# Optimization experiments

Hardware: AMD Instinct MI355X
Metric: run time of the kernel (lower is better)

## Reference

```python
import jax, jax.numpy as jnp
import numpy as np

N = 20000
E = 320000
LN_EPS = 1e-5
NEG_SLOPE = 0.2


def setup_inputs() -> dict:
    key = jax.random.key(0)
    ks = jax.random.split(key, 12)
    d = {}
    d['x'] = jax.random.normal(ks[0], (N, 512), dtype=jnp.float32)
    d['edge_index'] = jax.random.randint(ks[1], (2, E), 0, N, dtype=jnp.int64)
    s = 1.0 / np.sqrt(512.0)
    d['W1'] = jax.random.normal(ks[2], (512, 512), dtype=jnp.float32) * s
    d['a_src1'] = jax.random.normal(ks[3], (8, 64), dtype=jnp.float32) * s
    d['a_dst1'] = jax.random.normal(ks[4], (8, 64), dtype=jnp.float32) * s
    d['b1'] = jnp.zeros((512,), jnp.float32)
    d['g1'] = jnp.ones((512,), jnp.float32)
    d['beta1'] = jnp.zeros((512,), jnp.float32)
    d['W2'] = jax.random.normal(ks[5], (512, 512), dtype=jnp.float32) * s
    d['a_src2'] = jax.random.normal(ks[6], (1, 512), dtype=jnp.float32) * s
    d['a_dst2'] = jax.random.normal(ks[7], (1, 512), dtype=jnp.float32) * s
    d['b2'] = jnp.zeros((512,), jnp.float32)
    d['g2'] = jnp.ones((512,), jnp.float32)
    d['beta2'] = jnp.zeros((512,), jnp.float32)
    return d


def _segment_softmax(logits, seg, num_segments):
    # logits: [E, H]; softmax over edges sharing the same destination node
    m = jax.ops.segment_max(logits, seg, num_segments=num_segments)  # [N, H]
    e = jnp.exp(logits - m[seg])
    s = jax.ops.segment_sum(e, seg, num_segments=num_segments)  # [N, H]
    return e / s[seg]


def _gat_conv(x, src, dst, W, a_s, a_d, b, concat):
    # PyG GATConv (eval mode, self-loops already appended to src/dst)
    H, C = a_s.shape
    n = x.shape[0]
    h = (x @ W).reshape(n, H, C)                      # [N, H, C]
    alpha_s = jnp.einsum('nhc,hc->nh', h, a_s)        # [N, H]
    alpha_d = jnp.einsum('nhc,hc->nh', h, a_d)
    logits = jax.nn.leaky_relu(alpha_s[src] + alpha_d[dst], NEG_SLOPE)  # [E, H]
    alpha = _segment_softmax(logits, dst, n)          # [E, H]
    msg = h[src] * alpha[:, :, None]                  # [E, H, C]
    out = jax.ops.segment_sum(msg, dst, num_segments=n)  # [N, H, C]
    out = out.reshape(n, H * C) if concat else out.mean(axis=1)
    return out + b


def _layer_norm(x, g, beta):
    mu = jnp.mean(x, axis=-1, keepdims=True)
    var = jnp.var(x, axis=-1, keepdims=True)
    return (x - mu) * jax.lax.rsqrt(var + LN_EPS) * g + beta


def _forward(x, edge_index, W1, a_src1, a_dst1, b1, g1, beta1,
             W2, a_src2, a_dst2, b2, g2, beta2):
    n = x.shape[0]
    loops = jnp.arange(n, dtype=edge_index.dtype)
    src = jnp.concatenate([edge_index[0], loops])
    dst = jnp.concatenate([edge_index[1], loops])
    # layer 1: heads=8, concat
    x_new = _gat_conv(x, src, dst, W1, a_src1, a_dst1, b1, concat=True)
    x_new = jax.nn.elu(_layer_norm(x_new, g1, beta1))
    x = x + x_new  # 512 == 512 residual
    # layer 2: heads=1, mean (concat=False)
    x_new = _gat_conv(x, src, dst, W2, a_src2, a_dst2, b2, concat=False)
    x_new = jax.nn.elu(_layer_norm(x_new, g2, beta2))
    return x + x_new


def reference(x, edge_index, W1, a_src1, a_dst1, b1, g1, beta1,
              W2, a_src2, a_dst2, b2, g2, beta2):
    return _forward(x, edge_index, W1, a_src1, a_dst1, b1, g1, beta1,
                    W2, a_src2, a_dst2, b2, g2, beta2)
```

## Files before the change

kernel.cpp:

```cpp
#include <hip/hip_runtime.h>
#include <hip/hip_bf16.h>
#include <math.h>

#define NN 20000
#define NE 320000
#define DIM 512
#define LN_EPS 1e-5f
#define NEG_SLOPE 0.2f

typedef __attribute__((ext_vector_type(8))) short bf16x8;
typedef __attribute__((ext_vector_type(4))) float f32x4;
typedef __attribute__((ext_vector_type(4))) unsigned int u32x4;

__device__ inline void gload_lds16(const void* g, void* l) {
    __builtin_amdgcn_global_load_lds(
        (const __attribute__((address_space(1))) void*)g,
        (__attribute__((address_space(3))) void*)l, 16, 0, 0);
}

__device__ inline short f2bf(float f) {
    __hip_bfloat16 b = __float2bfloat16(f);
    return *reinterpret_cast<short*>(&b);
}


__global__ void count_k(const int* __restrict__ dst, int* __restrict__ cnt) {
    int e = blockIdx.x * blockDim.x + threadIdx.x;
    if (e < NE) {
        int d = dst[e];
        d = (d < 0) ? 0 : (d >= NN ? NN - 1 : d);
        atomicAdd(&cnt[d], 1);
    }
}

__global__ __launch_bounds__(1024) void scan_k(const int* __restrict__ cnt,
                                               int* __restrict__ off,
                                               int* __restrict__ cur) {
    __shared__ int s[1024];
    const int t = threadIdx.x;
    const int lo = t * 20;
    int loc[20];
    int sum = 0;
#pragma unroll
    for (int i = 0; i < 20; i++) {
        int idx = lo + i;
        int v = (idx < NN) ? cnt[idx] : 0;
        loc[i] = v; sum += v;
    }
    s[t] = sum;
    __syncthreads();
    for (int o = 1; o < 1024; o <<= 1) {
        int x = (t >= o) ? s[t - o] : 0;
        __syncthreads();
        s[t] += x;
        __syncthreads();
    }
    int run = s[t] - sum;
#pragma unroll
    for (int i = 0; i < 20; i++) {
        int idx = lo + i;
        if (idx < NN) { off[idx] = run; cur[idx] = run; run += loc[i]; }
    }
    if (t == 1023) off[NN] = s[1023];
}

__global__ void fill_k(const int* __restrict__ src, const int* __restrict__ dst,
                       int* __restrict__ cur, int* __restrict__ slot) {
    int e = blockIdx.x * blockDim.x + threadIdx.x;
    if (e < NE) {
        int d = dst[e];
        d = (d < 0) ? 0 : (d >= NN ? NN - 1 : d);
        int sv = src[e];
        sv = (sv < 0) ? 0 : (sv >= NN ? NN - 1 : sv);
        int p = atomicAdd(&cur[d], 1);
        slot[p] = sv;
    }
}


__global__ void conv_k(const float* __restrict__ in, __hip_bfloat16* __restrict__ out, int n) {
    int i = (blockIdx.x * blockDim.x + threadIdx.x) * 4;
    if (i < n) {
        float4 v = *(const float4*)&in[i];
        out[i + 0] = __float2bfloat16(v.x);
        out[i + 1] = __float2bfloat16(v.y);
        out[i + 2] = __float2bfloat16(v.z);
        out[i + 3] = __float2bfloat16(v.w);
    }
}

__global__ __launch_bounds__(256) void convT_k(const float* __restrict__ W1f,
                                               const float* __restrict__ W2f,
                                               __hip_bfloat16* __restrict__ B1,
                                               __hip_bfloat16* __restrict__ B2) {
    const float* W = blockIdx.z ? W2f : W1f;
    __hip_bfloat16* BT = blockIdx.z ? B2 : B1;
    __shared__ float tile[32][33];
    const int bk = blockIdx.x * 32, bn = blockIdx.y * 32;
    const int tx = threadIdx.x & 31, ty = threadIdx.x >> 5;
#pragma unroll
    for (int i = 0; i < 32; i += 8)
        tile[ty + i][tx] = W[(size_t)(bk + ty + i) * DIM + bn + tx];
    __syncthreads();
#pragma unroll
    for (int i = 0; i < 32; i += 8)
        BT[(size_t)(bn + ty + i) * DIM + bk + tx] = __float2bfloat16(tile[tx][ty + i]);
}

__global__ void sum8_k(const float* __restrict__ ps, const float* __restrict__ pd,
                       float* __restrict__ os, float* __restrict__ od) {
    int n = blockIdx.x * blockDim.x + threadIdx.x;
    if (n < NN) {
        float a = 0.f, b = 0.f;
#pragma unroll
        for (int k = 0; k < 8; k++) { a += ps[(size_t)k * NN + n]; b += pd[(size_t)k * NN + n]; }
        os[n] = a; od[n] = b;
    }
}


template <int H>
__global__ __launch_bounds__(256) void gemm_mfma(const short* __restrict__ A,
                                                 const short* __restrict__ BT,
                                                 __hip_bfloat16* __restrict__ C,
                                                 const float* __restrict__ a_s,
                                                 const float* __restrict__ a_d,
                                                 float* __restrict__ p_as,
                                                 float* __restrict__ p_ad,
                                                 int M) {
    __shared__ __align__(16) short SMEM[64 * 136];
    short* As = SMEM;
    short* Bs = SMEM + 4096;
    const int t = threadIdx.x;
    const int rowBase = blockIdx.y * 128;
    const int colBase = blockIdx.x * 128;
    const int wave = t >> 6, lane = t & 63;
    const int wr = (wave >> 1) * 64;
    const int wc = (wave & 1) * 64;
    const int quad = lane >> 4, l16 = lane & 15;

    f32x4 acc[4][4];
#pragma unroll
    for (int i = 0; i < 4; i++)
#pragma unroll
        for (int j = 0; j < 4; j++) acc[i][j] = f32x4{0.f, 0.f, 0.f, 0.f};

    const int srow = t >> 2;
    const int skof = (t & 3) * 8;
    int ar0 = rowBase + srow;       if (ar0 > M - 1) ar0 = M - 1;
    int ar1 = rowBase + 64 + srow;  if (ar1 > M - 1) ar1 = M - 1;
    const int bn0 = colBase + srow;
    const int bn1 = colBase + 64 + srow;

    for (int k0 = 0; k0 < DIM; k0 += 32) {
        gload_lds16(A + (size_t)ar0 * DIM + k0 + skof, As + t * 8);
        gload_lds16(A + (size_t)ar1 * DIM + k0 + skof, As + 2048 + t * 8);
        gload_lds16(BT + (size_t)bn0 * DIM + k0 + skof, Bs + t * 8);
        gload_lds16(BT + (size_t)bn1 * DIM + k0 + skof, Bs + 2048 + t * 8);
        __syncthreads();

        bf16x8 af[4], bfr[4];
#pragma unroll
        for (int i = 0; i < 4; i++)
            af[i] = *(const bf16x8*)&As[(wr + i * 16 + l16) * 32 + quad * 8];
#pragma unroll
        for (int j = 0; j < 4; j++)
            bfr[j] = *(const bf16x8*)&Bs[(wc + j * 16 + l16) * 32 + quad * 8];
#pragma unroll
        for (int i = 0; i < 4; i++)
#pragma unroll
            for (int j = 0; j < 4; j++)
                acc[i][j] = __builtin_amdgcn_mfma_f32_16x16x32_bf16(af[i], bfr[j], acc[i][j], 0, 0, 0);
        __syncthreads();
    }

#pragma unroll
    for (int p = 0; p < 2; p++) {
        if ((wave >> 1) == p) {
#pragma unroll
            for (int i = 0; i < 4; i++)
#pragma unroll
                for (int j = 0; j < 4; j++)
#pragma unroll
                    for (int r = 0; r < 4; r++)
                        SMEM[(i * 16 + quad * 4 + r) * 136 + wc + j * 16 + l16] =
                            f2bf(acc[i][j][r]);
        }
        __syncthreads();
#pragma unroll
        for (int k = 0; k < 4; k++) {
            const int row = k * 16 + (t >> 4);
            const int col = (t & 15) * 8;
            const int gr = rowBase + p * 64 + row;
            if (gr < M) {
                bf16x8 vv = *(const bf16x8*)&SMEM[row * 136 + col];
                *(bf16x8*)&C[(size_t)gr * DIM + colBase + col] = vv;
            }
        }
        __syncthreads();
    }

    const int slab = 2 * blockIdx.x + (wave & 1);
    const int cb = (H == 8) ? slab * 64 : (colBase + wc);
    float asc[4], adc[4];
#pragma unroll
    for (int j = 0; j < 4; j++) {
        asc[j] = a_s[cb + j * 16 + l16];
        adc[j] = a_d[cb + j * 16 + l16];
    }
#pragma unroll
    for (int i = 0; i < 4; i++) {
#pragma unroll
        for (int r = 0; r < 4; r++) {
            float vs = acc[i][0][r] * asc[0] + acc[i][1][r] * asc[1] +
                       acc[i][2][r] * asc[2] + acc[i][3][r] * asc[3];
            float vd = acc[i][0][r] * adc[0] + acc[i][1][r] * adc[1] +
                       acc[i][2][r] * adc[2] + acc[i][3][r] * adc[3];
#pragma unroll
            for (int o = 8; o; o >>= 1) { vs += __shfl_down(vs, o); vd += __shfl_down(vd, o); }
            if (l16 == 0) {
                const int row = rowBase + wr + i * 16 + quad * 4 + r;
                if (row < M) {
                    if (H == 8) {
                        p_as[(size_t)row * 8 + slab] = vs;
                        p_ad[(size_t)row * 8 + slab] = vd;
                    } else {
                        p_as[(size_t)slab * NN + row] = vs;
                        p_ad[(size_t)slab * NN + row] = vd;
                    }
                }
            }
        }
    }
}


template <int H>
__global__ __launch_bounds__(256) void agg_k(const __hip_bfloat16* __restrict__ h,
                                             const float* __restrict__ alp_s,
                                             const float* __restrict__ alp_d,
                                             const int* __restrict__ off,
                                             const int* __restrict__ slot,
                                             const float* __restrict__ bias,
                                             const float* __restrict__ gamma,
                                             const float* __restrict__ beta,
                                             const float* x_res,
                                             float* x_out,
                                             __hip_bfloat16* x_out_b) {
    const int wid = threadIdx.x >> 6;
    const int lane = threadIdx.x & 63;
    const int n = blockIdx.x * 4 + wid;
    const int head = (H == 8) ? (lane >> 3) : 0;

    const int o0 = off[n];
    const int deg = off[n + 1] - o0;
    const int total = deg + 1;

    const float ad = (H == 8) ? alp_d[(size_t)n * 8 + head] : alp_d[n];

    int v = 0x7fffffff;
    if (lane < total && lane < 64) v = (lane < deg) ? slot[o0 + lane] : n;
#pragma unroll
    for (int k = 2; k <= 64; k <<= 1) {
#pragma unroll
        for (int j = k >> 1; j > 0; j >>= 1) {
            int o = __shfl_xor(v, j);
            bool takeMin = (((lane & k) == 0) == ((lane & j) == 0));
            v = takeMin ? min(v, o) : max(v, o);
        }
    }
    const int nsort = (total < 64) ? total : 64;

    float acc[8];
#pragma unroll
    for (int r = 0; r < 8; r++) acc[r] = 0.f;
    float ld = 0.f;
    const unsigned short* hu = (const unsigned short*)h;

    auto zcomp = [&](int s) -> float {
        float z = ((H == 8) ? alp_s[(size_t)s * 8 + head] : alp_s[s]) + ad;
        return (z >= 0.f) ? z : NEG_SLOPE * z;
    };
    auto fmarow = [&](const u32x4& rv, float p) {
#pragma unroll
        for (int q = 0; q < 4; q++) {
            unsigned int u = rv[q];
            acc[2 * q]     += p * __uint_as_float(u << 16);
            acc[2 * q + 1] += p * __uint_as_float(u & 0xffff0000u);
        }
    };

    int e = 0;
    for (; e + 4 <= nsort; e += 4) {
        const int s0 = __shfl(v, e), s1 = __shfl(v, e + 1);
        const int s2 = __shfl(v, e + 2), s3 = __shfl(v, e + 3);
        const u32x4 r0 = *(const u32x4*)(hu + (size_t)s0 * DIM + lane * 8);
        const u32x4 r1 = *(const u32x4*)(hu + (size_t)s1 * DIM + lane * 8);
        const u32x4 r2 = *(const u32x4*)(hu + (size_t)s2 * DIM + lane * 8);
        const u32x4 r3 = *(const u32x4*)(hu + (size_t)s3 * DIM + lane * 8);
        const float z0 = zcomp(s0), z1 = zcomp(s1), z2 = zcomp(s2), z3 = zcomp(s3);
        const float p0 = __expf(z0), p1 = __expf(z1), p2 = __expf(z2), p3 = __expf(z3);
        ld += p0; fmarow(r0, p0);
        ld += p1; fmarow(r1, p1);
        ld += p2; fmarow(r2, p2);
        ld += p3; fmarow(r3, p3);
    }
    for (; e < nsort; e++) {
        const int s = __shfl(v, e);
        const u32x4 rv = *(const u32x4*)(hu + (size_t)s * DIM + lane * 8);
        const float p = __expf(zcomp(s));
        ld += p; fmarow(rv, p);
    }
    for (int e2 = 64; e2 < total; e2++) {
        const int s = (e2 < deg) ? slot[o0 + e2] : n;
        const u32x4 rv = *(const u32x4*)(hu + (size_t)s * DIM + lane * 8);
        const float p = __expf(zcomp(s));
        ld += p; fmarow(rv, p);
    }

    const float inv = 1.f / ld;
    const int c0 = lane * 8;
    const float4 ba = *(const float4*)&bias[c0];
    const float4 bb = *(const float4*)&bias[c0 + 4];
    float xn[8];
    xn[0] = acc[0] * inv + ba.x; xn[1] = acc[1] * inv + ba.y;
    xn[2] = acc[2] * inv + ba.z; xn[3] = acc[3] * inv + ba.w;
    xn[4] = acc[4] * inv + bb.x; xn[5] = acc[5] * inv + bb.y;
    xn[6] = acc[6] * inv + bb.z; xn[7] = acc[7] * inv + bb.w;

    float s1 = 0.f, s2 = 0.f;
#pragma unroll
    for (int r = 0; r < 8; r++) { s1 += xn[r]; s2 += xn[r] * xn[r]; }
#pragma unroll
    for (int o = 32; o; o >>= 1) { s1 += __shfl_xor(s1, o); s2 += __shfl_xor(s2, o); }
    const float mu = s1 * (1.f / DIM);
    const float rs = rsqrtf(s2 * (1.f / DIM) - mu * mu + LN_EPS);

    const float4 ga = *(const float4*)&gamma[c0];
    const float4 gb = *(const float4*)&gamma[c0 + 4];
    const float4 ea = *(const float4*)&beta[c0];
    const float4 eb = *(const float4*)&beta[c0 + 4];
    const float4 xa = *(const float4*)&x_res[(size_t)n * DIM + c0];
    const float4 xb = *(const float4*)&x_res[(size_t)n * DIM + c0 + 4];
    const float gv[8] = {ga.x, ga.y, ga.z, ga.w, gb.x, gb.y, gb.z, gb.w};
    const float ev[8] = {ea.x, ea.y, ea.z, ea.w, eb.x, eb.y, eb.z, eb.w};
    const float xv[8] = {xa.x, xa.y, xa.z, xa.w, xb.x, xb.y, xb.z, xb.w};

    float out[8];
#pragma unroll
    for (int r = 0; r < 8; r++) {
        float y = (xn[r] - mu) * rs * gv[r] + ev[r];
        y = (y > 0.f) ? y : expm1f(y);
        out[r] = xv[r] + y;
    }
    *(float4*)&x_out[(size_t)n * DIM + c0]     = make_float4(out[0], out[1], out[2], out[3]);
    *(float4*)&x_out[(size_t)n * DIM + c0 + 4] = make_float4(out[4], out[5], out[6], out[7]);
    if (x_out_b) {
        __hip_bfloat16 tb[8];
#pragma unroll
        for (int r = 0; r < 8; r++) tb[r] = __float2bfloat16(out[r]);
        *(bf16x8*)&x_out_b[(size_t)n * DIM + c0] = *(bf16x8*)tb;
    }
}


extern "C" void kernel_launch(void* const* d_in, const int* in_sizes, int n_in,
                              void* d_out, int out_size, void* d_ws, size_t ws_size,
                              hipStream_t stream) {
    const float* x = (const float*)d_in[0];
    const int* ei = (const int*)d_in[1];
    const float* W1 = (const float*)d_in[2];
    const float* as1 = (const float*)d_in[3];
    const float* ad1 = (const float*)d_in[4];
    const float* b1 = (const float*)d_in[5];
    const float* g1 = (const float*)d_in[6];
    const float* be1 = (const float*)d_in[7];
    const float* W2 = (const float*)d_in[8];
    const float* as2 = (const float*)d_in[9];
    const float* ad2 = (const float*)d_in[10];
    const float* b2 = (const float*)d_in[11];
    const float* g2 = (const float*)d_in[12];
    const float* be2 = (const float*)d_in[13];
    float* out = (float*)d_out;

    char* ws = (char*)d_ws;
    size_t o = 0;
    auto alloc = [&](size_t bytes) { size_t r = o; o += (bytes + 255) & ~(size_t)255; return r; };
    int* p_cnt = (int*)(ws + alloc((size_t)NN * 4));
    int* p_off = (int*)(ws + alloc((size_t)(NN + 1) * 4));
    int* p_cur = (int*)(ws + alloc((size_t)NN * 4));
    int* p_slot = (int*)(ws + alloc((size_t)NE * 4));
    __hip_bfloat16* p_hb = (__hip_bfloat16*)(ws + alloc((size_t)NN * DIM * 2));
    __hip_bfloat16* p_xb = (__hip_bfloat16*)(ws + alloc((size_t)NN * DIM * 2));
    __hip_bfloat16* p_bt1 = (__hip_bfloat16*)(ws + alloc((size_t)DIM * DIM * 2));
    __hip_bfloat16* p_bt2 = (__hip_bfloat16*)(ws + alloc((size_t)DIM * DIM * 2));
    float* p_as = (float*)(ws + alloc((size_t)NN * 8 * 4));
    float* p_ad = (float*)(ws + alloc((size_t)NN * 8 * 4));
    float* p_as2 = (float*)(ws + alloc((size_t)NN * 4));
    float* p_ad2 = (float*)(ws + alloc((size_t)NN * 4));
    float* p_x1 = out;

    const int* e_src = ei;
    const int* e_dst = ei + NE;

    hipMemsetAsync(p_cnt, 0, (size_t)NN * 4, stream);
    count_k<<<(NE + 255) / 256, 256, 0, stream>>>(e_dst, p_cnt);
    scan_k<<<1, 1024, 0, stream>>>(p_cnt, p_off, p_cur);
    fill_k<<<(NE + 255) / 256, 256, 0, stream>>>(e_src, e_dst, p_cur, p_slot);

    const int NX = NN * DIM;
    dim3 ggrid(4, (NN + 127) / 128);

    convT_k<<<dim3(16, 16, 2), 256, 0, stream>>>(W1, W2, p_bt1, p_bt2);
    conv_k<<<(NX / 4 + 255) / 256, 256, 0, stream>>>(x, p_xb, NX);

    gemm_mfma<8><<<ggrid, 256, 0, stream>>>((const short*)p_xb, (const short*)p_bt1, p_hb,
                                            as1, ad1, p_as, p_ad, NN);
    agg_k<8><<<NN / 4, 256, 0, stream>>>(p_hb, p_as, p_ad, p_off, p_slot, b1, g1, be1,
                                         x, p_x1, p_xb);

    gemm_mfma<1><<<ggrid, 256, 0, stream>>>((const short*)p_xb, (const short*)p_bt2, p_hb,
                                            as2, ad2, p_as, p_ad, NN);
    sum8_k<<<(NN + 255) / 256, 256, 0, stream>>>(p_as, p_ad, p_as2, p_ad2);
    agg_k<1><<<NN / 4, 256, 0, stream>>>(p_hb, p_as2, p_ad2, p_off, p_slot, b2, g2, be2,
                                         p_x1, out, nullptr);
}
```

Baseline: 340.9 us.

## Switch intermediates from bf16 to fp16 and double-buffer GEMM LDS tiles

Converts every bf16 intermediate (x, weights, h, residual copy) to fp16 and swaps the bf16 MFMA for the fp16 MFMA. The GEMM k-loop gets two LDS buffers, so the next K slice is loaded while the current one is computed. Precision changes from bf16 to fp16 (more mantissa, less range), and the aggregation kernel now unpacks fp16 with conversions rather than bit shifts. The fp16 MFMA has the same shape and throughput as the bf16 one, so the gain has to come from overlapping loads with compute in the GEMM.

After: 357.0 us. 1.05x slower.

```diff
diff --git a/kernel.cpp b/kernel.cpp
--- a/kernel.cpp
+++ b/kernel.cpp
@@ -1,5 +1,6 @@
 #include <hip/hip_runtime.h>
 #include <hip/hip_bf16.h>
+#include <hip/hip_fp16.h>
 #include <math.h>
 
 #define NN 20000
@@ -8,7 +9,8 @@
 #define LN_EPS 1e-5f
 #define NEG_SLOPE 0.2f
 
-typedef __attribute__((ext_vector_type(8))) short bf16x8;
+typedef __attribute__((ext_vector_type(8))) short s16x8;
+typedef __attribute__((ext_vector_type(8))) _Float16 f16x8;
 typedef __attribute__((ext_vector_type(4))) float f32x4;
 typedef __attribute__((ext_vector_type(4))) unsigned int u32x4;
 
@@ -18,9 +20,9 @@
         (__attribute__((address_space(3))) void*)l, 16, 0, 0);
 }
 
-__device__ inline short f2bf(float f) {
-    __hip_bfloat16 b = __float2bfloat16(f);
-    return *reinterpret_cast<short*>(&b);
+__device__ inline unsigned short f2h(float f) {
+    __half h = __float2half(f);
+    return *reinterpret_cast<unsigned short*>(&h);
 }
 
 
@@ -78,23 +80,23 @@
 }
 
 
-__global__ void conv_k(const float* __restrict__ in, __hip_bfloat16* __restrict__ out, int n) {
+__global__ void conv_k(const float* __restrict__ in, unsigned short* __restrict__ out, int n) {
     int i = (blockIdx.x * blockDim.x + threadIdx.x) * 4;
     if (i < n) {
         float4 v = *(const float4*)&in[i];
-        out[i + 0] = __float2bfloat16(v.x);
-        out[i + 1] = __float2bfloat16(v.y);
-        out[i + 2] = __float2bfloat16(v.z);
-        out[i + 3] = __float2bfloat16(v.w);
+        out[i + 0] = f2h(v.x);
+        out[i + 1] = f2h(v.y);
+        out[i + 2] = f2h(v.z);
+        out[i + 3] = f2h(v.w);
     }
 }
 
 __global__ __launch_bounds__(256) void convT_k(const float* __restrict__ W1f,
                                                const float* __restrict__ W2f,
-                                               __hip_bfloat16* __restrict__ B1,
-                                               __hip_bfloat16* __restrict__ B2) {
+                                               unsigned short* __restrict__ B1,
+                                               unsigned short* __restrict__ B2) {
     const float* W = blockIdx.z ? W2f : W1f;
-    __hip_bfloat16* BT = blockIdx.z ? B2 : B1;
+    unsigned short* BT = blockIdx.z ? B2 : B1;
     __shared__ float tile[32][33];
     const int bk = blockIdx.x * 32, bn = blockIdx.y * 32;
     const int tx = threadIdx.x & 31, ty = threadIdx.x >> 5;
@@ -104,7 +106,7 @@
     __syncthreads();
 #pragma unroll
     for (int i = 0; i < 32; i += 8)
-        BT[(size_t)(bn + ty + i) * DIM + bk + tx] = __float2bfloat16(tile[tx][ty + i]);
+        BT[(size_t)(bn + ty + i) * DIM + bk + tx] = f2h(tile[tx][ty + i]);
 }
 
 __global__ void sum8_k(const float* __restrict__ ps, const float* __restrict__ pd,
@@ -122,15 +124,17 @@
 template <int H>
 __global__ __launch_bounds__(256) void gemm_mfma(const short* __restrict__ A,
                                                  const short* __restrict__ BT,
-                                                 __hip_bfloat16* __restrict__ C,
+                                                 unsigned short* __restrict__ C,
                                                  const float* __restrict__ a_s,
                                                  const float* __restrict__ a_d,
                                                  float* __restrict__ p_as,
                                                  float* __restrict__ p_ad,
                                                  int M) {
-    __shared__ __align__(16) short SMEM[64 * 136];
-    short* As = SMEM;
-    short* Bs = SMEM + 4096;
+    __shared__ __align__(16) short SMEM[16384];
+    short* As0 = SMEM;
+    short* Bs0 = SMEM + 4096;
+    short* As1 = SMEM + 8192;
+    short* Bs1 = SMEM + 12288;
     const int t = threadIdx.x;
     const int rowBase = blockIdx.y * 128;
     const int colBase = blockIdx.x * 128;
@@ -152,25 +156,39 @@
     const int bn0 = colBase + srow;
     const int bn1 = colBase + 64 + srow;
 
-    for (int k0 = 0; k0 < DIM; k0 += 32) {
+    auto stage = [&](int k0, short* As, short* Bs) {
         gload_lds16(A + (size_t)ar0 * DIM + k0 + skof, As + t * 8);
         gload_lds16(A + (size_t)ar1 * DIM + k0 + skof, As + 2048 + t * 8);
         gload_lds16(BT + (size_t)bn0 * DIM + k0 + skof, Bs + t * 8);
         gload_lds16(BT + (size_t)bn1 * DIM + k0 + skof, Bs + 2048 + t * 8);
-        __syncthreads();
-
-        bf16x8 af[4], bfr[4];
+    };
+    auto compute = [&](const short* As, const short* Bs) {
+        f16x8 af[4], bfr[4];
+#pragma unroll
+        for (int i = 0; i < 4; i++) {
+            s16x8 tmp = *(const s16x8*)&As[(wr + i * 16 + l16) * 32 + quad * 8];
+            af[i] = __builtin_bit_cast(f16x8, tmp);
+        }
+#pragma unroll
+        for (int j = 0; j < 4; j++) {
+            s16x8 tmp = *(const s16x8*)&Bs[(wc + j * 16 + l16) * 32 + quad * 8];
+            bfr[j] = __builtin_bit_cast(f16x8, tmp);
+        }
 #pragma unroll
         for (int i = 0; i < 4; i++)
-            af[i] = *(const bf16x8*)&As[(wr + i * 16 + l16) * 32 + quad * 8];
-#pragma unroll
-        for (int j = 0; j < 4; j++)
-            bfr[j] = *(const bf16x8*)&Bs[(wc + j * 16 + l16) * 32 + quad * 8];
-#pragma unroll
-        for (int i = 0; i < 4; i++)
 #pragma unroll
             for (int j = 0; j < 4; j++)
-                acc[i][j] = __builtin_amdgcn_mfma_f32_16x16x32_bf16(af[i], bfr[j], acc[i][j], 0, 0, 0);
+                acc[i][j] = __builtin_amdgcn_mfma_f32_16x16x32_f16(af[i], bfr[j], acc[i][j], 0, 0, 0);
+    };
+
+    stage(0, As0, Bs0);
+    __syncthreads();
+    for (int k0 = 0; k0 < DIM; k0 += 64) {
+        if (k0 + 32 < DIM) stage(k0 + 32, As1, Bs1);
+        compute(As0, Bs0);
+        __syncthreads();
+        if (k0 + 64 < DIM) stage(k0 + 64, As0, Bs0);
+        compute(As1, Bs1);
         __syncthreads();
     }
 
@@ -184,7 +202,7 @@
 #pragma unroll
                     for (int r = 0; r < 4; r++)
                         SMEM[(i * 16 + quad * 4 + r) * 136 + wc + j * 16 + l16] =
-                            f2bf(acc[i][j][r]);
+                            (short)f2h(acc[i][j][r]);
         }
         __syncthreads();
 #pragma unroll
@@ -193,8 +211,8 @@
             const int col = (t & 15) * 8;
             const int gr = rowBase + p * 64 + row;
             if (gr < M) {
-                bf16x8 vv = *(const bf16x8*)&SMEM[row * 136 + col];
-                *(bf16x8*)&C[(size_t)gr * DIM + colBase + col] = vv;
+                s16x8 vv = *(const s16x8*)&SMEM[row * 136 + col];
+                *(s16x8*)&C[(size_t)gr * DIM + colBase + col] = vv;
             }
         }
         __syncthreads();
@@ -236,7 +254,7 @@
 
 
 template <int H>
-__global__ __launch_bounds__(256) void agg_k(const __hip_bfloat16* __restrict__ h,
+__global__ __launch_bounds__(256) void agg_k(const unsigned short* __restrict__ h,
                                              const float* __restrict__ alp_s,
                                              const float* __restrict__ alp_d,
                                              const int* __restrict__ off,
@@ -246,7 +264,7 @@
                                              const float* __restrict__ beta,
                                              const float* x_res,
                                              float* x_out,
-                                             __hip_bfloat16* x_out_b) {
+                                             unsigned short* x_out_b) {
     const int wid = threadIdx.x >> 6;
     const int lane = threadIdx.x & 63;
     const int n = blockIdx.x * 4 + wid;
@@ -275,19 +293,16 @@
 #pragma unroll
     for (int r = 0; r < 8; r++) acc[r] = 0.f;
     float ld = 0.f;
-    const unsigned short* hu = (const unsigned short*)h;
+    const unsigned short* hu = h;
 
     auto zcomp = [&](int s) -> float {
         float z = ((H == 8) ? alp_s[(size_t)s * 8 + head] : alp_s[s]) + ad;
         return (z >= 0.f) ? z : NEG_SLOPE * z;
     };
     auto fmarow = [&](const u32x4& rv, float p) {
-#pragma unroll
-        for (int q = 0; q < 4; q++) {
-            unsigned int u = rv[q];
-            acc[2 * q]     += p * __uint_as_float(u << 16);
-            acc[2 * q + 1] += p * __uint_as_float(u & 0xffff0000u);
-        }
+        f16x8 hv = __builtin_bit_cast(f16x8, rv);
+#pragma unroll
+        for (int r = 0; r < 8; r++) acc[r] = fmaf((float)hv[r], p, acc[r]);
     };
 
     int e = 0;
@@ -298,8 +313,8 @@
         const u32x4 r1 = *(const u32x4*)(hu + (size_t)s1 * DIM + lane * 8);
         const u32x4 r2 = *(const u32x4*)(hu + (size_t)s2 * DIM + lane * 8);
         const u32x4 r3 = *(const u32x4*)(hu + (size_t)s3 * DIM + lane * 8);
-        const float z0 = zcomp(s0), z1 = zcomp(s1), z2 = zcomp(s2), z3 = zcomp(s3);
-        const float p0 = __expf(z0), p1 = __expf(z1), p2 = __expf(z2), p3 = __expf(z3);
+        const float p0 = __expf(zcomp(s0)), p1 = __expf(zcomp(s1));
+        const float p2 = __expf(zcomp(s2)), p3 = __expf(zcomp(s3));
         ld += p0; fmarow(r0, p0);
         ld += p1; fmarow(r1, p1);
         ld += p2; fmarow(r2, p2);
@@ -356,10 +371,10 @@
     *(float4*)&x_out[(size_t)n * DIM + c0]     = make_float4(out[0], out[1], out[2], out[3]);
     *(float4*)&x_out[(size_t)n * DIM + c0 + 4] = make_float4(out[4], out[5], out[6], out[7]);
     if (x_out_b) {
-        __hip_bfloat16 tb[8];
-#pragma unroll
-        for (int r = 0; r < 8; r++) tb[r] = __float2bfloat16(out[r]);
-        *(bf16x8*)&x_out_b[(size_t)n * DIM + c0] = *(bf16x8*)tb;
+        unsigned short tb[8];
+#pragma unroll
+        for (int r = 0; r < 8; r++) tb[r] = f2h(out[r]);
+        *(s16x8*)&x_out_b[(size_t)n * DIM + c0] = *(s16x8*)tb;
     }
 }
 
@@ -390,10 +405,10 @@
     int* p_off = (int*)(ws + alloc((size_t)(NN + 1) * 4));
     int* p_cur = (int*)(ws + alloc((size_t)NN * 4));
     int* p_slot = (int*)(ws + alloc((size_t)NE * 4));
-    __hip_bfloat16* p_hb = (__hip_bfloat16*)(ws + alloc((size_t)NN * DIM * 2));
-    __hip_bfloat16* p_xb = (__hip_bfloat16*)(ws + alloc((size_t)NN * DIM * 2));
-    __hip_bfloat16* p_bt1 = (__hip_bfloat16*)(ws + alloc((size_t)DIM * DIM * 2));
-    __hip_bfloat16* p_bt2 = (__hip_bfloat16*)(ws + alloc((size_t)DIM * DIM * 2));
+    unsigned short* p_hb = (unsigned short*)(ws + alloc((size_t)NN * DIM * 2));
+    unsigned short* p_xb = (unsigned short*)(ws + alloc((size_t)NN * DIM * 2));
+    unsigned short* p_bt1 = (unsigned short*)(ws + alloc((size_t)DIM * DIM * 2));
+    unsigned short* p_bt2 = (unsigned short*)(ws + alloc((size_t)DIM * DIM * 2));
     float* p_as = (float*)(ws + alloc((size_t)NN * 8 * 4));
     float* p_ad = (float*)(ws + alloc((size_t)NN * 8 * 4));
     float* p_as2 = (float*)(ws + alloc((size_t)NN * 4));
```

## Double-buffer GEMM LDS tiles, shrink row tile to 64, use atomics for attention logits

Applied to the files above, without the earlier changes.

The GEMM is restructured to use 64x128 tiles with each wave owning a 64x32 column strip. A/B K-slices are double-buffered in LDS so global loads overlap MFMA compute. Attention dot products are now accumulated with atomicAdd into zeroed buffers, which removes the separate sum8 reduction kernel for layer 2. This doubles the grid size and halves per-wave MFMA work. It adds memsets and atomic traffic, and makes the summation order nondeterministic.

Measured after the change: 379.9 us. 1.11x slower.

```diff
diff --git a/kernel.cpp b/kernel.cpp
--- a/kernel.cpp
+++ b/kernel.cpp
@@ -107,17 +107,6 @@
         BT[(size_t)(bn + ty + i) * DIM + bk + tx] = __float2bfloat16(tile[tx][ty + i]);
 }
 
-__global__ void sum8_k(const float* __restrict__ ps, const float* __restrict__ pd,
-                       float* __restrict__ os, float* __restrict__ od) {
-    int n = blockIdx.x * blockDim.x + threadIdx.x;
-    if (n < NN) {
-        float a = 0.f, b = 0.f;
-#pragma unroll
-        for (int k = 0; k < 8; k++) { a += ps[(size_t)k * NN + n]; b += pd[(size_t)k * NN + n]; }
-        os[n] = a; od[n] = b;
-    }
-}
-
 
 template <int H>
 __global__ __launch_bounds__(256) void gemm_mfma(const short* __restrict__ A,
@@ -128,106 +117,100 @@
                                                  float* __restrict__ p_as,
                                                  float* __restrict__ p_ad,
                                                  int M) {
-    __shared__ __align__(16) short SMEM[64 * 136];
-    short* As = SMEM;
-    short* Bs = SMEM + 4096;
+    __shared__ __align__(16) short SMEM[12288];
+    short* As0 = SMEM;
+    short* Bs0 = SMEM + 2048;
+    short* As1 = SMEM + 6144;
+    short* Bs1 = SMEM + 8192;
     const int t = threadIdx.x;
-    const int rowBase = blockIdx.y * 128;
+    const int rowBase = blockIdx.y * 64;
     const int colBase = blockIdx.x * 128;
     const int wave = t >> 6, lane = t & 63;
-    const int wr = (wave >> 1) * 64;
-    const int wc = (wave & 1) * 64;
+    const int wc = wave * 32;
     const int quad = lane >> 4, l16 = lane & 15;
 
-    f32x4 acc[4][4];
+    f32x4 acc[4][2];
 #pragma unroll
     for (int i = 0; i < 4; i++)
 #pragma unroll
-        for (int j = 0; j < 4; j++) acc[i][j] = f32x4{0.f, 0.f, 0.f, 0.f};
+        for (int j = 0; j < 2; j++) acc[i][j] = f32x4{0.f, 0.f, 0.f, 0.f};
 
     const int srow = t >> 2;
     const int skof = (t & 3) * 8;
-    int ar0 = rowBase + srow;       if (ar0 > M - 1) ar0 = M - 1;
-    int ar1 = rowBase + 64 + srow;  if (ar1 > M - 1) ar1 = M - 1;
+    int ar = rowBase + srow;  if (ar > M - 1) ar = M - 1;
     const int bn0 = colBase + srow;
     const int bn1 = colBase + 64 + srow;
 
-    for (int k0 = 0; k0 < DIM; k0 += 32) {
-        gload_lds16(A + (size_t)ar0 * DIM + k0 + skof, As + t * 8);
-        gload_lds16(A + (size_t)ar1 * DIM + k0 + skof, As + 2048 + t * 8);
+    auto stage = [&](int k0, short* As, short* Bs) {
+        gload_lds16(A + (size_t)ar * DIM + k0 + skof, As + t * 8);
         gload_lds16(BT + (size_t)bn0 * DIM + k0 + skof, Bs + t * 8);
         gload_lds16(BT + (size_t)bn1 * DIM + k0 + skof, Bs + 2048 + t * 8);
+    };
+    auto compute = [&](const short* As, const short* Bs) {
+        bf16x8 af[4], bfr[2];
+#pragma unroll
+        for (int i = 0; i < 4; i++)
+            af[i] = *(const bf16x8*)&As[(i * 16 + l16) * 32 + quad * 8];
+#pragma unroll
+        for (int j = 0; j < 2; j++)
+            bfr[j] = *(const bf16x8*)&Bs[(wc + j * 16 + l16) * 32 + quad * 8];
+#pragma unroll
+        for (int i = 0; i < 4; i++)
+#pragma unroll
+            for (int j = 0; j < 2; j++)
+                acc[i][j] = __builtin_amdgcn_mfma_f32_16x16x32_bf16(af[i], bfr[j], acc[i][j], 0, 0, 0);
+    };
+
+    stage(0, As0, Bs0);
+    __syncthreads();
+    for (int k0 = 0; k0 < DIM; k0 += 64) {
+        if (k0 + 32 < DIM) stage(k0 + 32, As1, Bs1);
+        compute(As0, Bs0);
         __syncthreads();
-
-        bf16x8 af[4], bfr[4];
-#pragma unroll
-        for (int i = 0; i < 4; i++)
-            af[i] = *(const bf16x8*)&As[(wr + i * 16 + l16) * 32 + quad * 8];
-#pragma unroll
-        for (int j = 0; j < 4; j++)
-            bfr[j] = *(const bf16x8*)&Bs[(wc + j * 16 + l16) * 32 + quad * 8];
-#pragma unroll
-        for (int i = 0; i < 4; i++)
-#pragma unroll
-            for (int j = 0; j < 4; j++)
-                acc[i][j] = __builtin_amdgcn_mfma_f32_16x16x32_bf16(af[i], bfr[j], acc[i][j], 0, 0, 0);
+        if (k0 + 64 < DIM) stage(k0 + 64, As0, Bs0);
+        compute(As1, Bs1);
         __syncthreads();
     }
 
 #pragma unroll
-    for (int p = 0; p < 2; p++) {
-        if ((wave >> 1) == p) {
-#pragma unroll
-            for (int i = 0; i < 4; i++)
-#pragma unroll
-                for (int j = 0; j < 4; j++)
-#pragma unroll
-                    for (int r = 0; r < 4; r++)
-                        SMEM[(i * 16 + quad * 4 + r) * 136 + wc + j * 16 + l16] =
-                            f2bf(acc[i][j][r]);
+    for (int i = 0; i < 4; i++)
+#pragma unroll
+        for (int j = 0; j < 2; j++)
+#pragma unroll
+            for (int r = 0; r < 4; r++)
+                SMEM[(i * 16 + quad * 4 + r) * 136 + wc + j * 16 + l16] = f2bf(acc[i][j][r]);
+    __syncthreads();
+#pragma unroll
+    for (int k = 0; k < 4; k++) {
+        const int row = k * 16 + (t >> 4);
+        const int col = (t & 15) * 8;
+        const int gr = rowBase + row;
+        if (gr < M) {
+            bf16x8 vv = *(const bf16x8*)&SMEM[row * 136 + col];
+            *(bf16x8*)&C[(size_t)gr * DIM + colBase + col] = vv;
         }
-        __syncthreads();
-#pragma unroll
-        for (int k = 0; k < 4; k++) {
-            const int row = k * 16 + (t >> 4);
-            const int col = (t & 15) * 8;
-            const int gr = rowBase + p * 64 + row;
-            if (gr < M) {
-                bf16x8 vv = *(const bf16x8*)&SMEM[row * 136 + col];
-                *(bf16x8*)&C[(size_t)gr * DIM + colBase + col] = vv;
-            }
-        }
-        __syncthreads();
-    }
-
-    const int slab = 2 * blockIdx.x + (wave & 1);
-    const int cb = (H == 8) ? slab * 64 : (colBase + wc);
-    float asc[4], adc[4];
-#pragma unroll
-    for (int j = 0; j < 4; j++) {
-        asc[j] = a_s[cb + j * 16 + l16];
-        adc[j] = a_d[cb + j * 16 + l16];
+    }
+
+    const int head = (H == 8) ? (2 * blockIdx.x + (wave >> 1)) : 0;
+    float asc[2], adc[2];
+#pragma unroll
+    for (int j = 0; j < 2; j++) {
+        asc[j] = a_s[colBase + wc + j * 16 + l16];
+        adc[j] = a_d[colBase + wc + j * 16 + l16];
     }
 #pragma unroll
     for (int i = 0; i < 4; i++) {
 #pragma unroll
         for (int r = 0; r < 4; r++) {
-            float vs = acc[i][0][r] * asc[0] + acc[i][1][r] * asc[1] +
-                       acc[i][2][r] * asc[2] + acc[i][3][r] * asc[3];
-            float vd = acc[i][0][r] * adc[0] + acc[i][1][r] * adc[1] +
-                       acc[i][2][r] * adc[2] + acc[i][3][r] * adc[3];
+            float vs = acc[i][0][r] * asc[0] + acc[i][1][r] * asc[1];
+            float vd = acc[i][0][r] * adc[0] + acc[i][1][r] * adc[1];
 #pragma unroll
             for (int o = 8; o; o >>= 1) { vs += __shfl_down(vs, o); vd += __shfl_down(vd, o); }
             if (l16 == 0) {
-                const int row = rowBase + wr + i * 16 + quad * 4 + r;
+                const int row = rowBase + i * 16 + quad * 4 + r;
                 if (row < M) {
-                    if (H == 8) {
-                        p_as[(size_t)row * 8 + slab] = vs;
-                        p_ad[(size_t)row * 8 + slab] = vd;
-                    } else {
-                        p_as[(size_t)slab * NN + row] = vs;
-                        p_ad[(size_t)slab * NN + row] = vd;
-                    }
+                    atomicAdd(&p_as[(size_t)row * H + head], vs);
+                    atomicAdd(&p_ad[(size_t)row * H + head], vd);
                 }
             }
         }
@@ -396,8 +379,6 @@
     __hip_bfloat16* p_bt2 = (__hip_bfloat16*)(ws + alloc((size_t)DIM * DIM * 2));
     float* p_as = (float*)(ws + alloc((size_t)NN * 8 * 4));
     float* p_ad = (float*)(ws + alloc((size_t)NN * 8 * 4));
-    float* p_as2 = (float*)(ws + alloc((size_t)NN * 4));
-    float* p_ad2 = (float*)(ws + alloc((size_t)NN * 4));
     float* p_x1 = out;
 
     const int* e_src = ei;
@@ -409,19 +390,22 @@
     fill_k<<<(NE + 255) / 256, 256, 0, stream>>>(e_src, e_dst, p_cur, p_slot);
 
     const int NX = NN * DIM;
-    dim3 ggrid(4, (NN + 127) / 128);
+    dim3 ggrid(4, (NN + 63) / 64);
 
     convT_k<<<dim3(16, 16, 2), 256, 0, stream>>>(W1, W2, p_bt1, p_bt2);
     conv_k<<<(NX / 4 + 255) / 256, 256, 0, stream>>>(x, p_xb, NX);
 
+    hipMemsetAsync(p_as, 0, (size_t)NN * 8 * 4, stream);
+    hipMemsetAsync(p_ad, 0, (size_t)NN * 8 * 4, stream);
     gemm_mfma<8><<<ggrid, 256, 0, stream>>>((const short*)p_xb, (const short*)p_bt1, p_hb,
                                             as1, ad1, p_as, p_ad, NN);
     agg_k<8><<<NN / 4, 256, 0, stream>>>(p_hb, p_as, p_ad, p_off, p_slot, b1, g1, be1,
                                          x, p_x1, p_xb);
 
+    hipMemsetAsync(p_as, 0, (size_t)NN * 4, stream);
+    hipMemsetAsync(p_ad, 0, (size_t)NN * 4, stream);
     gemm_mfma<1><<<ggrid, 256, 0, stream>>>((const short*)p_xb, (const short*)p_bt2, p_hb,
                                             as2, ad2, p_as, p_ad, NN);
-    sum8_k<<<(NN + 255) / 256, 256, 0, stream>>>(p_as, p_ad, p_as2, p_ad2);
-    agg_k<1><<<NN / 4, 256, 0, stream>>>(p_hb, p_as2, p_ad2, p_off, p_slot, b2, g2, be2,
+    agg_k<1><<<NN / 4, 256, 0, stream>>>(p_hb, p_as, p_ad, p_off, p_slot, b2, g2, be2,
                                          p_x1, out, nullptr);
 }
```

## Double GEMM K-tile to 64 and XOR-swizzle LDS layout

Applied to the files above, without the earlier changes.

The bf16 MFMA GEMM now stages a K-slice of 64 per iteration instead of 32, which halves the number of barrier pairs per block. The LDS tiles use an XOR swizzle on 16-byte chunks, keyed on the row index, to avoid bank conflicts when waves read fragments. LDS use grows to 32 KB per block, which may reduce occupancy. Each thread now issues four async loads per operand per stage.

Result: slower. 352.3 us (+3.3%).

```diff
diff --git a/kernel.cpp b/kernel.cpp
--- a/kernel.cpp
+++ b/kernel.cpp
@@ -128,9 +128,9 @@
                                                  float* __restrict__ p_as,
                                                  float* __restrict__ p_ad,
                                                  int M) {
-    __shared__ __align__(16) short SMEM[64 * 136];
+    __shared__ __align__(16) short SMEM[16384];
     short* As = SMEM;
-    short* Bs = SMEM + 4096;
+    short* Bs = SMEM + 8192;
     const int t = threadIdx.x;
     const int rowBase = blockIdx.y * 128;
     const int colBase = blockIdx.x * 128;
@@ -145,32 +145,42 @@
 #pragma unroll
         for (int j = 0; j < 4; j++) acc[i][j] = f32x4{0.f, 0.f, 0.f, 0.f};
 
-    const int srow = t >> 2;
-    const int skof = (t & 3) * 8;
-    int ar0 = rowBase + srow;       if (ar0 > M - 1) ar0 = M - 1;
-    int ar1 = rowBase + 64 + srow;  if (ar1 > M - 1) ar1 = M - 1;
-    const int bn0 = colBase + srow;
-    const int bn1 = colBase + 64 + srow;
-
-    for (int k0 = 0; k0 < DIM; k0 += 32) {
-        gload_lds16(A + (size_t)ar0 * DIM + k0 + skof, As + t * 8);
-        gload_lds16(A + (size_t)ar1 * DIM + k0 + skof, As + 2048 + t * 8);
-        gload_lds16(BT + (size_t)bn0 * DIM + k0 + skof, Bs + t * 8);
-        gload_lds16(BT + (size_t)bn1 * DIM + k0 + skof, Bs + 2048 + t * 8);
-        __syncthreads();
-
+    auto stage = [&](int k0) {
+#pragma unroll
+        for (int i = 0; i < 4; i++) {
+            const int s = t + 256 * i;
+            const int row = s >> 3;
+            const int col = 8 * ((s & 7) ^ (row & 7));
+            int arow = rowBase + row; if (arow > M - 1) arow = M - 1;
+            gload_lds16(A + (size_t)arow * DIM + k0 + col, As + 8 * s);
+            const int brow = colBase + row;
+            gload_lds16(BT + (size_t)brow * DIM + k0 + col, Bs + 8 * s);
+        }
+    };
+    auto compute = [&](int kk) {
         bf16x8 af[4], bfr[4];
 #pragma unroll
-        for (int i = 0; i < 4; i++)
-            af[i] = *(const bf16x8*)&As[(wr + i * 16 + l16) * 32 + quad * 8];
-#pragma unroll
-        for (int j = 0; j < 4; j++)
-            bfr[j] = *(const bf16x8*)&Bs[(wc + j * 16 + l16) * 32 + quad * 8];
+        for (int i = 0; i < 4; i++) {
+            const int row = wr + i * 16 + l16;
+            af[i] = *(const bf16x8*)&As[row * 64 + ((kk * 32 + quad * 8) ^ ((row & 7) << 3))];
+        }
+#pragma unroll
+        for (int j = 0; j < 4; j++) {
+            const int row = wc + j * 16 + l16;
+            bfr[j] = *(const bf16x8*)&Bs[row * 64 + ((kk * 32 + quad * 8) ^ ((row & 7) << 3))];
+        }
 #pragma unroll
         for (int i = 0; i < 4; i++)
 #pragma unroll
             for (int j = 0; j < 4; j++)
                 acc[i][j] = __builtin_amdgcn_mfma_f32_16x16x32_bf16(af[i], bfr[j], acc[i][j], 0, 0, 0);
+    };
+
+    for (int k0 = 0; k0 < DIM; k0 += 64) {
+        stage(k0);
+        __syncthreads();
+        compute(0);
+        compute(1);
         __syncthreads();
     }
 
```
